# Kernel tuning notes

Measured on AMD Instinct MI355X. Metric: run time of the kernel, lower is better.

## Reference

```python
import jax, jax.numpy as jnp
import numpy as np

PLANE_AXES = jnp.array([[[0., 1., 0.], [1., 0., 0.], [0., 0., 1.]],
                        [[0., 0., 1.], [1., 0., 0.], [0., 1., 0.]],
                        [[0., 1., 0.], [0., 0., 1.], [1., 0., 0.]]], dtype=jnp.float32)


def setup_inputs() -> dict:
    key = jax.random.key(0)
    k1, k2 = jax.random.split(key)
    M, C, R = 1048576, 32, 512
    coords = jax.random.uniform(k1, (M, 3), jnp.float32, -1.0, 1.0)
    triplane = jax.random.normal(k2, (1, 3, C, R, R), jnp.float32) * 0.1
    return {"coords": coords, "triplane": triplane}


def _bilinear_sample(plane, x, y):
    # plane: [C, R, R]; x, y: [M] pixel coords (align_corners=True mapping applied).
    # Matches torch grid_sample(mode='bilinear', padding_mode='zeros', align_corners=True).
    R = plane.shape[-1]
    x0 = jnp.floor(x)
    y0 = jnp.floor(y)
    x0i = x0.astype(jnp.int32)
    y0i = y0.astype(jnp.int32)
    wx1 = x - x0
    wx0 = 1.0 - wx1
    wy1 = y - y0
    wy0 = 1.0 - wy1

    def tap(xi, yi, w):
        valid = ((xi >= 0) & (xi < R) & (yi >= 0) & (yi < R)).astype(plane.dtype)
        xc = jnp.clip(xi, 0, R - 1)
        yc = jnp.clip(yi, 0, R - 1)
        return plane[:, yc, xc] * (w * valid)  # [C, M]

    return (tap(x0i, y0i, wx0 * wy0) + tap(x0i + 1, y0i, wx1 * wy0)
            + tap(x0i, y0i + 1, wx0 * wy1) + tap(x0i + 1, y0i + 1, wx1 * wy1))


def reference(coords, triplane):
    # coords: [M, 3]; triplane: [1, 3, C, R, R]
    _, P, C, R, _ = triplane.shape
    planes = jnp.clip(triplane.reshape(P, C, R, R), -1.0, 1.0)
    inv = jnp.linalg.inv(PLANE_AXES)  # [3, 3, 3]
    # project_onto_planes: bmm(coords, inv_planes), keep first two coords (x, y)
    proj = jnp.einsum('mc,pcd->pmd', coords, inv)[..., :2]  # [3, M, 2]
    px = (proj[..., 0] + 1.0) * 0.5 * (R - 1)  # align_corners=True
    py = (proj[..., 1] + 1.0) * 0.5 * (R - 1)
    feat = jax.vmap(_bilinear_sample)(planes, px, py)  # [3, C, M]
    return feat.sum(0).T  # [M, C] — sum across the 3 planes
```

## Files before the change

### kernel.cpp

```cpp
#include <hip/hip_runtime.h>
#include <hip/hip_bf16.h>
#include <stdint.h>

#define RES 512
#define CH  32
#define NP  3
#define NTEX (NP * RES * RES)
#define WS_BYTES ((size_t)NTEX * CH * sizeof(uint16_t))

static __device__ __forceinline__ uint16_t f2bf(float f) {
    union { float f; uint32_t u; } v; v.f = f;
    uint32_t u = v.u;
    uint32_t r = (u + 0x7fffu + ((u >> 16) & 1u)) >> 16;
    return (uint16_t)r;
}

__global__ __launch_bounds__(256) void k_transpose(const float* __restrict__ tri,
                                                   uint16_t* __restrict__ ws) {
    int t = blockIdx.x * 256 + threadIdx.x;
    if (t >= NTEX) return;
    int x = t & (RES - 1);
    int y = (t >> 9) & (RES - 1);
    int p = t >> 18;
    const float* src = tri + (size_t)p * CH * RES * RES + (size_t)y * RES + x;
    uint32_t packed[16];
#pragma unroll
    for (int i = 0; i < 16; ++i) {
        float f0 = src[(size_t)(2 * i + 0) * (RES * RES)];
        float f1 = src[(size_t)(2 * i + 1) * (RES * RES)];
        f0 = fminf(1.f, fmaxf(-1.f, f0));
        f1 = fminf(1.f, fmaxf(-1.f, f1));
        packed[i] = (uint32_t)f2bf(f0) | ((uint32_t)f2bf(f1) << 16);
    }
    uint4* dst = (uint4*)(ws + (size_t)t * CH);
#pragma unroll
    for (int i = 0; i < 4; ++i)
        dst[i] = make_uint4(packed[4 * i], packed[4 * i + 1], packed[4 * i + 2], packed[4 * i + 3]);
}

__global__ __launch_bounds__(256) void k_gather(const float* __restrict__ coords,
                                                const uint16_t* __restrict__ ws,
                                                float* __restrict__ out, int M) {
    int m = blockIdx.x * 256 + threadIdx.x;
    if (m >= M) return;
    float cx = coords[3 * m + 0];
    float cy = coords[3 * m + 1];
    float cz = coords[3 * m + 2];

    float acc[CH];
#pragma unroll
    for (int c = 0; c < CH; ++c) acc[c] = 0.f;

    float us[3] = {cy, cz, cy};
    float vs[3] = {cx, cx, cz};

#pragma unroll
    for (int p = 0; p < 3; ++p) {
        float px = (us[p] + 1.f) * (0.5f * (RES - 1));
        float py = (vs[p] + 1.f) * (0.5f * (RES - 1));
        float x0f = floorf(px), y0f = floorf(py);
        int x0 = (int)x0f, y0 = (int)y0f;
        float wx1 = px - x0f, wx0 = 1.f - wx1;
        float wy1 = py - y0f, wy0 = 1.f - wy1;
        int   xs[2]  = {x0, x0 + 1};
        int   ys[2]  = {y0, y0 + 1};
        float wxv[2] = {wx0, wx1};
        float wyv[2] = {wy0, wy1};
#pragma unroll
        for (int j = 0; j < 2; ++j) {
#pragma unroll
            for (int i = 0; i < 2; ++i) {
                int xi = xs[i], yi = ys[j];
                bool valid = (xi >= 0) & (xi < RES) & (yi >= 0) & (yi < RES);
                int xc = min(max(xi, 0), RES - 1);
                int yc = min(max(yi, 0), RES - 1);
                float w = valid ? (wxv[i] * wyv[j]) : 0.f;
                const uint4* tp = (const uint4*)(ws + (((size_t)p * RES + yc) * RES + xc) * CH);
#pragma unroll
                for (int q = 0; q < 4; ++q) {
                    uint4 d = tp[q];
                    uint32_t wwv[4] = {d.x, d.y, d.z, d.w};
#pragma unroll
                    for (int e = 0; e < 4; ++e) {
                        union { uint32_t u; float f; } lo, hi;
                        lo.u = wwv[e] << 16;
                        hi.u = wwv[e] & 0xffff0000u;
                        acc[q * 8 + 2 * e + 0] += w * lo.f;
                        acc[q * 8 + 2 * e + 1] += w * hi.f;
                    }
                }
            }
        }
    }

    float4* dst = (float4*)(out + (size_t)m * CH);
#pragma unroll
    for (int i = 0; i < 8; ++i)
        dst[i] = make_float4(acc[4 * i], acc[4 * i + 1], acc[4 * i + 2], acc[4 * i + 3]);
}

__global__ __launch_bounds__(256) void k_gather_direct(const float* __restrict__ coords,
                                                       const float* __restrict__ tri,
                                                       float* __restrict__ out, int M) {
    int m = blockIdx.x * 256 + threadIdx.x;
    if (m >= M) return;
    float cx = coords[3 * m + 0];
    float cy = coords[3 * m + 1];
    float cz = coords[3 * m + 2];
    float acc[CH];
#pragma unroll
    for (int c = 0; c < CH; ++c) acc[c] = 0.f;
    float us[3] = {cy, cz, cy};
    float vs[3] = {cx, cx, cz};
    for (int p = 0; p < 3; ++p) {
        float px = (us[p] + 1.f) * (0.5f * (RES - 1));
        float py = (vs[p] + 1.f) * (0.5f * (RES - 1));
        float x0f = floorf(px), y0f = floorf(py);
        int x0 = (int)x0f, y0 = (int)y0f;
        float wx1 = px - x0f, wx0 = 1.f - wx1;
        float wy1 = py - y0f, wy0 = 1.f - wy1;
        int   xs[2]  = {x0, x0 + 1};
        int   ys[2]  = {y0, y0 + 1};
        float wxv[2] = {wx0, wx1};
        float wyv[2] = {wy0, wy1};
        for (int j = 0; j < 2; ++j)
            for (int i = 0; i < 2; ++i) {
                int xi = xs[i], yi = ys[j];
                bool valid = (xi >= 0) & (xi < RES) & (yi >= 0) & (yi < RES);
                int xc = min(max(xi, 0), RES - 1);
                int yc = min(max(yi, 0), RES - 1);
                float w = valid ? (wxv[i] * wyv[j]) : 0.f;
                const float* base = tri + ((size_t)p * CH) * RES * RES + (size_t)yc * RES + xc;
#pragma unroll
                for (int c = 0; c < CH; ++c) {
                    float v = base[(size_t)c * RES * RES];
                    v = fminf(1.f, fmaxf(-1.f, v));
                    acc[c] += w * v;
                }
            }
    }
    float4* dst = (float4*)(out + (size_t)m * CH);
#pragma unroll
    for (int i = 0; i < 8; ++i)
        dst[i] = make_float4(acc[4 * i], acc[4 * i + 1], acc[4 * i + 2], acc[4 * i + 3]);
}

extern "C" void kernel_launch(void* const* d_in, const int* in_sizes, int n_in,
                              void* d_out, int out_size, void* d_ws, size_t ws_size,
                              hipStream_t stream) {
    const float* coords = (const float*)d_in[0];
    const float* tri    = (const float*)d_in[1];
    float* out          = (float*)d_out;
    int M = in_sizes[0] / 3;

    if (ws_size >= WS_BYTES) {
        uint16_t* ws = (uint16_t*)d_ws;
        k_transpose<<<(NTEX + 255) / 256, 256, 0, stream>>>(tri, ws);
        k_gather<<<(M + 255) / 256, 256, 0, stream>>>(coords, ws, out, M);
    } else {
        k_gather_direct<<<(M + 255) / 256, 256, 0, stream>>>(coords, tri, out, M);
    }
}
```

Measured before the change: 434.8 us.

## Split each gather point across four lanes and vectorize transpose loads

The gather kernel now assigns four threads per sample point, each handling 8 channels with one 16-byte load per tap, instead of one thread loading 64 bytes per tap for all 32 channels. Neighbouring lanes therefore read contiguous texel data and write contiguous output, which cuts per-thread registers and should improve coalescing and occupancy. Output stores become nontemporal to avoid polluting cache. The transpose kernel processes two texels per thread using float2 loads. The cost is that coordinate loading and weight computation are repeated in all four lanes of a point.

```diff
diff --git a/kernel.cpp b/kernel.cpp
--- a/kernel.cpp
+++ b/kernel.cpp
@@ -6,7 +6,10 @@
 #define CH  32
 #define NP  3
 #define NTEX (NP * RES * RES)
+#define NT2  (NTEX / 2)
 #define WS_BYTES ((size_t)NTEX * CH * sizeof(uint16_t))
+
+typedef float vfloat4 __attribute__((ext_vector_type(4)));
 
 static __device__ __forceinline__ uint16_t f2bf(float f) {
     union { float f; uint32_t u; } v; v.f = f;
@@ -17,39 +20,48 @@
 
 __global__ __launch_bounds__(256) void k_transpose(const float* __restrict__ tri,
                                                    uint16_t* __restrict__ ws) {
-    int t = blockIdx.x * 256 + threadIdx.x;
-    if (t >= NTEX) return;
-    int x = t & (RES - 1);
-    int y = (t >> 9) & (RES - 1);
-    int p = t >> 18;
+    int t2 = blockIdx.x * 256 + threadIdx.x;
+    if (t2 >= NT2) return;
+    int xp = t2 & (RES / 2 - 1);
+    int y  = (t2 >> 8) & (RES - 1);
+    int p  = t2 >> 17;
+    int x  = xp * 2;
     const float* src = tri + (size_t)p * CH * RES * RES + (size_t)y * RES + x;
-    uint32_t packed[16];
+    uint32_t pa[16], pb[16];
 #pragma unroll
     for (int i = 0; i < 16; ++i) {
-        float f0 = src[(size_t)(2 * i + 0) * (RES * RES)];
-        float f1 = src[(size_t)(2 * i + 1) * (RES * RES)];
-        f0 = fminf(1.f, fmaxf(-1.f, f0));
-        f1 = fminf(1.f, fmaxf(-1.f, f1));
-        packed[i] = (uint32_t)f2bf(f0) | ((uint32_t)f2bf(f1) << 16);
+        float2 f0 = *(const float2*)&src[(size_t)(2 * i + 0) * (RES * RES)];
+        float2 f1 = *(const float2*)&src[(size_t)(2 * i + 1) * (RES * RES)];
+        float a0 = fminf(1.f, fmaxf(-1.f, f0.x));
+        float a1 = fminf(1.f, fmaxf(-1.f, f1.x));
+        float b0 = fminf(1.f, fmaxf(-1.f, f0.y));
+        float b1 = fminf(1.f, fmaxf(-1.f, f1.y));
+        pa[i] = (uint32_t)f2bf(a0) | ((uint32_t)f2bf(a1) << 16);
+        pb[i] = (uint32_t)f2bf(b0) | ((uint32_t)f2bf(b1) << 16);
     }
-    uint4* dst = (uint4*)(ws + (size_t)t * CH);
+    uint4* dst = (uint4*)(ws + (size_t)(2 * t2) * CH);
 #pragma unroll
     for (int i = 0; i < 4; ++i)
-        dst[i] = make_uint4(packed[4 * i], packed[4 * i + 1], packed[4 * i + 2], packed[4 * i + 3]);
+        dst[i] = make_uint4(pa[4 * i], pa[4 * i + 1], pa[4 * i + 2], pa[4 * i + 3]);
+#pragma unroll
+    for (int i = 0; i < 4; ++i)
+        dst[4 + i] = make_uint4(pb[4 * i], pb[4 * i + 1], pb[4 * i + 2], pb[4 * i + 3]);
 }
 
 __global__ __launch_bounds__(256) void k_gather(const float* __restrict__ coords,
                                                 const uint16_t* __restrict__ ws,
                                                 float* __restrict__ out, int M) {
-    int m = blockIdx.x * 256 + threadIdx.x;
+    int tid = threadIdx.x;
+    int sub = tid & 3;
+    int m = blockIdx.x * 64 + (tid >> 2);
     if (m >= M) return;
     float cx = coords[3 * m + 0];
     float cy = coords[3 * m + 1];
     float cz = coords[3 * m + 2];
 
-    float acc[CH];
+    float acc[8];
 #pragma unroll
-    for (int c = 0; c < CH; ++c) acc[c] = 0.f;
+    for (int c = 0; c < 8; ++c) acc[c] = 0.f;
 
     float us[3] = {cy, cz, cy};
     float vs[3] = {cx, cx, cz};
@@ -75,28 +87,27 @@
                 int xc = min(max(xi, 0), RES - 1);
                 int yc = min(max(yi, 0), RES - 1);
                 float w = valid ? (wxv[i] * wyv[j]) : 0.f;
-                const uint4* tp = (const uint4*)(ws + (((size_t)p * RES + yc) * RES + xc) * CH);
+                const uint4* tp = (const uint4*)(ws + (((size_t)p * RES + yc) * RES + xc) * CH
+                                                 + (size_t)sub * 8);
+                uint4 d = *tp;
+                uint32_t vv[4] = {d.x, d.y, d.z, d.w};
 #pragma unroll
-                for (int q = 0; q < 4; ++q) {
-                    uint4 d = tp[q];
-                    uint32_t wwv[4] = {d.x, d.y, d.z, d.w};
-#pragma unroll
-                    for (int e = 0; e < 4; ++e) {
-                        union { uint32_t u; float f; } lo, hi;
-                        lo.u = wwv[e] << 16;
-                        hi.u = wwv[e] & 0xffff0000u;
-                        acc[q * 8 + 2 * e + 0] += w * lo.f;
-                        acc[q * 8 + 2 * e + 1] += w * hi.f;
-                    }
+                for (int e = 0; e < 4; ++e) {
+                    union { uint32_t u; float f; } lo, hi;
+                    lo.u = vv[e] << 16;
+                    hi.u = vv[e] & 0xffff0000u;
+                    acc[2 * e + 0] += w * lo.f;
+                    acc[2 * e + 1] += w * hi.f;
                 }
             }
         }
     }
 
-    float4* dst = (float4*)(out + (size_t)m * CH);
-#pragma unroll
-    for (int i = 0; i < 8; ++i)
-        dst[i] = make_float4(acc[4 * i], acc[4 * i + 1], acc[4 * i + 2], acc[4 * i + 3]);
+    vfloat4* dst = (vfloat4*)(out + (size_t)m * CH + (size_t)sub * 8);
+    vfloat4 v0 = {acc[0], acc[1], acc[2], acc[3]};
+    vfloat4 v1 = {acc[4], acc[5], acc[6], acc[7]};
+    __builtin_nontemporal_store(v0, dst);
+    __builtin_nontemporal_store(v1, dst + 1);
 }
 
 __global__ __launch_bounds__(256) void k_gather_direct(const float* __restrict__ coords,
@@ -155,8 +166,8 @@
 
     if (ws_size >= WS_BYTES) {
         uint16_t* ws = (uint16_t*)d_ws;
-        k_transpose<<<(NTEX + 255) / 256, 256, 0, stream>>>(tri, ws);
-        k_gather<<<(M + 255) / 256, 256, 0, stream>>>(coords, ws, out, M);
+        k_transpose<<<(NT2 + 255) / 256, 256, 0, stream>>>(tri, ws);
+        k_gather<<<(M + 63) / 64, 256, 0, stream>>>(coords, ws, out, M);
     } else {
         k_gather_direct<<<(M + 255) / 256, 256, 0, stream>>>(coords, tri, out, M);
     }
```

Measured after the change: 406.3 us. 6.5% less time.
